# Performance work log

Hardware: AMD Instinct MI355X
Metric: run time of the kernel (lower is better)

## Reference

```python
import jax, jax.numpy as jnp
import numpy as np

N = 2048        # nodes
IN_DIM = 128    # input feature dim
K = 8           # channels
D = 32          # per-channel dim (C_dim)
ITERS = 4       # routing iterations
BETA = 1.0      # attention temperature
EPS = 1e-12     # F.normalize eps


def l2norm(x):
    # F.normalize(x, dim=-1): x / max(||x||_2, eps)
    n = jnp.linalg.norm(x, axis=-1, keepdims=True)
    return x / jnp.maximum(n, EPS)


def setup_inputs() -> dict:
    key = jax.random.key(0)
    k1, k2, k3, k4 = jax.random.split(key, 4)
    adj = jax.random.randint(k1, (N, N), 0, 2, dtype=jnp.int32)
    features = jax.random.normal(k2, (N, IN_DIM), dtype=jnp.float32)
    # parameters initialized ~ N(0,1) as in init_parameters
    W = jax.random.normal(k3, (K, IN_DIM, D), dtype=jnp.float32)
    b = jax.random.normal(k4, (K, D), dtype=jnp.float32)
    return {"adj": adj, "features": features, "W": W, "b": b}


def reference(adj, features, W, b):
    mask = (adj > 0)[None, :, :]                         # [1, N, N]
    # per-channel projection + row L2 normalize -> Z: [K, N, D]
    Z = l2norm(jnp.einsum('nd,kdc->knc', features, W) + b[:, None, :])
    for _ in range(ITERS):
        # per-channel masked attention scores [K, N, N]
        att = jnp.einsum('knc,kmc->knm', Z, Z)
        att = jnp.where(mask, att, 0.0) / BETA
        # softmax across channels (dim=2 in torch after cat == K axis here)
        att = jax.nn.softmax(att, axis=0)
        att = jnp.where(mask, att, 0.0)
        # weighted aggregate + residual + L2 normalize
        Z = l2norm(Z + jnp.einsum('knm,kmc->knc', att, Z))
    # concat channels along feature dim -> [N, K*D]
    return jnp.transpose(Z, (1, 0, 2)).reshape(N, K * D)
```

## Files before the change

### kernel.cpp

```cpp
#include <hip/hip_runtime.h>
#include <hip/hip_bf16.h>
#include <hip/hip_fp16.h>

#define NN 2048
#define KK 8
#define DD 32
#define ZSZ (KK * NN * DD)

#define TW(row, slot) (((row) << 4) + ((((slot) ^ (((row) >> 1) & 3))) << 2))
#define TW2(row, wo) (((row) << 4) + (((((wo) >> 2) ^ (((row) >> 1) & 3))) << 2) + ((wo) & 3))

typedef __attribute__((ext_vector_type(8))) short short8;
typedef __attribute__((ext_vector_type(4))) short short4v;
typedef __attribute__((ext_vector_type(4))) float f32x4;
typedef __attribute__((ext_vector_type(4))) unsigned int u32x4;

union UU { u32x4 q; short8 v; unsigned int u[4]; };
union U2 { uint2 q; short4v v; unsigned int u[2]; };

__device__ __forceinline__ unsigned int bfr(float x) {
  unsigned int u = __float_as_uint(x);
  return (u + 0x7fffu + ((u >> 16) & 1u)) >> 16;
}
__device__ __forceinline__ float bf2f(unsigned int h) {
  return __uint_as_float(h << 16);
}
__device__ __forceinline__ unsigned int packp(float a, float b) {
  union { __hip_bfloat162 h; unsigned int u; } cv;
  cv.h = __float22bfloat162_rn(make_float2(a, b));
  return cv.u;
}
__device__ __forceinline__ f32x4 MF(short8 a, short8 b, f32x4 c) {
  return __builtin_amdgcn_mfma_f32_16x16x32_bf16(a, b, c, 0, 0, 0);
}
__device__ __forceinline__ f32x4 MF16(short4v a, short4v b, f32x4 c) {
  return __builtin_amdgcn_mfma_f32_16x16x16bf16_1k(a, b, c, 0, 0, 0);
}
__device__ __forceinline__ short8 as_s8(u32x4 x) { UU u; u.q = x; return u.v; }

__global__ __launch_bounds__(256) void pm_kernel(const float* __restrict__ feat,
                                                 const float* __restrict__ W,
                                                 const float* __restrict__ bias,
                                                 unsigned short* __restrict__ Zghi,
                                                 unsigned short* __restrict__ Zthi,
                                                 const int* __restrict__ adj,
                                                 unsigned int* __restrict__ mbits) {
  __shared__ float fsh[1024];
  const int t = threadIdx.x;
  if (blockIdx.x < 256) {
    const int nb = blockIdx.x * 8;
    const int k = t >> 5, c = t & 31;
    *(float4*)&fsh[4 * t] = *(const float4*)&feat[nb * 128 + 4 * t];
    float s[8];
#pragma unroll
    for (int j = 0; j < 8; ++j) s[j] = bias[k * DD + c];
    const float* w = W + (k * 128) * DD + c;
    __syncthreads();
#pragma unroll 4
    for (int d = 0; d < 128; ++d) {
      float wv = w[d * DD];
#pragma unroll
      for (int j = 0; j < 8; ++j) s[j] = fmaf(fsh[j * 128 + d], wv, s[j]);
    }
    unsigned int hi[8];
#pragma unroll
    for (int j = 0; j < 8; ++j) {
      float sq = s[j] * s[j];
#pragma unroll
      for (int off = 16; off > 0; off >>= 1) sq += __shfl_xor(sq, off, 32);
      float z = s[j] / fmaxf(sqrtf(sq), 1e-12f);
      hi[j] = bfr(z);
      Zghi[(k * NN + nb + j) * DD + c] = (unsigned short)hi[j];
    }
    uint4 tp = make_uint4(hi[0] | (hi[1] << 16), hi[2] | (hi[3] << 16),
                          hi[4] | (hi[5] << 16), hi[6] | (hi[7] << 16));
    *(uint4*)&Zthi[(size_t)k * DD * NN + (size_t)c * NN + nb] = tp;
  } else {
    const int base = (blockIdx.x - 256) * 1024 + t;
    const int lane = t & 63;
    int v[4];
#pragma unroll
    for (int rr = 0; rr < 4; ++rr) v[rr] = adj[base + 256 * rr];
#pragma unroll
    for (int rr = 0; rr < 4; ++rr) {
      int idx = base + 256 * rr;
      unsigned long long b = __ballot(v[rr] > 0);
      if (lane == 0) mbits[idx >> 5] = (unsigned int)b;
      if (lane == 32) mbits[idx >> 5] = (unsigned int)(b >> 32);
    }
  }
}

template <int NCt>
__global__ __launch_bounds__(256) void rp_kernel(const __half* __restrict__ part,
                                                 unsigned short* __restrict__ Zghi,
                                                 unsigned short* __restrict__ Zthi) {
  __shared__ unsigned short T[DD][33];
  const int t = threadIdx.x;
  const int k = blockIdx.x >> 6, mt = blockIdx.x & 63;
  const int m0 = mt * 32;
  const int mloc = t >> 3, c4 = t & 7;
  const size_t idx = (size_t)(k * NN + m0 + mloc) * DD + 4 * c4;
  uint2 zb = *(const uint2*)&Zghi[idx];
  float4 v;
  v.x = bf2f(zb.x & 0xffffu);
  v.y = __uint_as_float(zb.x & 0xffff0000u);
  v.z = bf2f(zb.y & 0xffffu);
  v.w = __uint_as_float(zb.y & 0xffff0000u);
#pragma unroll
  for (int j = 0; j < NCt; ++j) {
    const __half2* ph = (const __half2*)&part[(size_t)j * ZSZ + idx];
    float2 a = __half22float2(ph[0]);
    float2 b = __half22float2(ph[1]);
    v.x += a.x; v.y += a.y; v.z += b.x; v.w += b.y;
  }
  float sq = v.x * v.x + v.y * v.y + v.z * v.z + v.w * v.w;
  sq += __shfl_xor(sq, 1, 8);
  sq += __shfl_xor(sq, 2, 8);
  sq += __shfl_xor(sq, 4, 8);
  const float sc = 1.0f / fmaxf(sqrtf(sq), 1e-12f);
  float z[4] = {v.x * sc, v.y * sc, v.z * sc, v.w * sc};
  unsigned int hi[4];
#pragma unroll
  for (int e = 0; e < 4; ++e) {
    hi[e] = bfr(z[e]);
    T[4 * c4 + e][mloc] = (unsigned short)hi[e];
  }
  *(uint2*)&Zghi[idx] = make_uint2(hi[0] | (hi[1] << 16), hi[2] | (hi[3] << 16));
  __syncthreads();
  const int cloc = t >> 3, m4 = t & 7;
  unsigned int o0 = (unsigned int)T[cloc][4 * m4 + 0] | ((unsigned int)T[cloc][4 * m4 + 1] << 16);
  unsigned int o1 = (unsigned int)T[cloc][4 * m4 + 2] | ((unsigned int)T[cloc][4 * m4 + 3] << 16);
  *(uint2*)&Zthi[(size_t)k * DD * NN + (size_t)cloc * NN + m0 + 4 * m4] = make_uint2(o0, o1);
}

template <int NS>
__global__ __launch_bounds__(256, 2) void iter_kernel(const unsigned short* __restrict__ Zghi,
                                                      const unsigned short* __restrict__ Zthi,
                                                      const unsigned int* __restrict__ mbits,
                                                      __half* __restrict__ part) {
  __shared__ __align__(16) unsigned int lds[2][8192];
  const int t = threadIdx.x;
  const int w = t >> 6;
  const int lane = t & 63;
  const int l15 = lane & 15;
  const int g = lane >> 4;
  const int nw = blockIdx.x * 64 + w * 16;
  const int mchunk = blockIdx.y * (NS * 32);

  const unsigned int* Zg = (const unsigned int*)Zghi;
  const unsigned int* Zt = (const unsigned int*)Zthi;

  short8 A[KK];
#pragma unroll
  for (int k = 0; k < KK; ++k)
    A[k] = as_s8(*(const u32x4*)&Zg[(size_t)(k * NN + nw + l15) * 16 + 4 * g]);

  unsigned int mword[NS];
#pragma unroll
  for (int q4 = 0; q4 < NS / 4; ++q4) {
    uint4 m4 = *(const uint4*)&mbits[(size_t)(nw + l15) * 64 + (mchunk >> 5) + 4 * q4];
    mword[4 * q4 + 0] = m4.x; mword[4 * q4 + 1] = m4.y;
    mword[4 * q4 + 2] = m4.z; mword[4 * q4 + 3] = m4.w;
  }

  f32x4 O[KK][2];
#pragma unroll
  for (int k = 0; k < KK; ++k)
#pragma unroll
    for (int ch = 0; ch < 2; ++ch) O[k][ch] = {0.0f, 0.0f, 0.0f, 0.0f};

  const int sqd = t & 3;
  const int sr0 = t >> 2;

  u32x4 Lgh[4], Lth[4];
  auto do_loads = [&](int mb) {
#pragma unroll
    for (int j = 0; j < 4; ++j) {
      int r = 64 * j + sr0;
      int k = r >> 5, rm = r & 31;
      Lgh[j] = *(const u32x4*)&Zg[(size_t)k * (NN * 16) + (size_t)(mb + rm) * 16 + sqd * 4];
      Lth[j] = *(const u32x4*)&Zt[(size_t)k * (NN * 16) + (size_t)rm * (NN / 2) + (mb >> 1) + sqd * 4];
    }
  };
  auto wr = [&](int buf) {
#pragma unroll
    for (int j = 0; j < 4; ++j) {
      int r = 64 * j + sr0;
      *(u32x4*)&lds[buf][TW(r, sqd)] = Lgh[j];
      *(u32x4*)&lds[buf][4096 + TW(r, sqd)] = Lth[j];
    }
  };

  do_loads(mchunk);
  wr(0);
  if (NS > 1) do_loads(mchunk + 32);
  __syncthreads();

#pragma unroll
  for (int st = 0; st < NS; ++st) {
    const unsigned int* B = lds[st & 1];
    if (st + 1 < NS) wr((st + 1) & 1);
    if (st + 2 < NS) do_loads(mchunk + (st + 2) * 32);

    const unsigned int mw = mword[st];
#pragma unroll
    for (int sub = 0; sub < 2; ++sub) {
      f32x4 S[KK];
#pragma unroll
      for (int k = 0; k < KK; ++k) {
        u32x4 bh = *(const u32x4*)&B[TW(k * 32 + 16 * sub + l15, g)];
        f32x4 z = {0.0f, 0.0f, 0.0f, 0.0f};
        S[k] = MF(as_s8(bh), A[k], z);
      }
#pragma unroll
      for (int r = 0; r < 4; ++r) {
        float e[KK];
        float sum = 0.0f;
#pragma unroll
        for (int k = 0; k < KK; ++k) { e[k] = __expf(S[k][r]); sum += e[k]; }
        float f = ((mw >> (16 * sub + 4 * g + r)) & 1u) ? __builtin_amdgcn_rcpf(sum) : 0.0f;
#pragma unroll
        for (int k = 0; k < KK; ++k) S[k][r] = e[k] * f;
      }
#pragma unroll
      for (int k = 0; k < KK; ++k) {
        U2 pa;
        pa.u[0] = packp(S[k][0], S[k][1]);
        pa.u[1] = packp(S[k][2], S[k][3]);
#pragma unroll
        for (int ch = 0; ch < 2; ++ch) {
          int row = k * 32 + 16 * ch + l15;
          U2 bv;
          bv.q = *(const uint2*)&B[4096 + TW2(row, 8 * sub + 2 * g)];
          O[k][ch] = MF16(pa.v, bv.v, O[k][ch]);
        }
      }
    }
    __syncthreads();
  }

  __half* dst = part + (size_t)blockIdx.y * ZSZ;
#pragma unroll
  for (int k = 0; k < KK; ++k)
#pragma unroll
    for (int ch = 0; ch < 2; ++ch) {
      f32x4 o = O[k][ch];
#pragma unroll
      for (int r = 0; r < 4; ++r)
        dst[(size_t)(k * NN + nw + 4 * g + r) * DD + 16 * ch + l15] = __float2half_rn(o[r]);
    }
}

template <int NCt>
__global__ __launch_bounds__(256) void ro_kernel(const unsigned short* __restrict__ Zghi,
                                                 const __half* __restrict__ part,
                                                 float* __restrict__ out) {
  const int n = blockIdx.x, t = threadIdx.x;
  const int k = t >> 5, c = t & 31;
  const size_t idx = (size_t)(k * NN + n) * DD + c;
  float v = bf2f((unsigned int)Zghi[idx]);
#pragma unroll
  for (int j = 0; j < NCt; ++j) v += __half2float(part[(size_t)j * ZSZ + idx]);
  float sq = v * v;
#pragma unroll
  for (int off = 16; off > 0; off >>= 1) sq += __shfl_xor(sq, off, 32);
  out[n * (KK * DD) + t] = v / fmaxf(sqrtf(sq), 1e-12f);
}

extern "C" void kernel_launch(void* const* d_in, const int* in_sizes, int n_in,
                              void* d_out, int out_size, void* d_ws, size_t ws_size,
                              hipStream_t stream) {
  const int* adj = (const int*)d_in[0];
  const float* feat = (const float*)d_in[1];
  const float* W = (const float*)d_in[2];
  const float* b = (const float*)d_in[3];
  float* out = (float*)d_out;

  int NC = 16;
  while (NC > 4) {
    size_t need = (size_t)ZSZ * 2 * 2 + (size_t)NN * 64 * 4 + (size_t)NC * ZSZ * 2;
    if (need <= ws_size) break;
    NC >>= 1;
  }

  unsigned short* Zghi = (unsigned short*)d_ws;
  unsigned short* Zthi = Zghi + ZSZ;
  unsigned int* mbits = (unsigned int*)(Zthi + ZSZ);
  __half* part = (__half*)(mbits + NN * 64);

  pm_kernel<<<256 + 4096, 256, 0, stream>>>(feat, W, b, Zghi, Zthi, adj, mbits);

  for (int it = 0; it < 4; ++it) {
    if (NC == 16)
      iter_kernel<4><<<dim3(32, 16), 256, 0, stream>>>(Zghi, Zthi, mbits, part);
    else if (NC == 8)
      iter_kernel<8><<<dim3(32, 8), 256, 0, stream>>>(Zghi, Zthi, mbits, part);
    else
      iter_kernel<16><<<dim3(32, 4), 256, 0, stream>>>(Zghi, Zthi, mbits, part);
    if (it < 3) {
      if (NC == 16)
        rp_kernel<16><<<512, 256, 0, stream>>>(part, Zghi, Zthi);
      else if (NC == 8)
        rp_kernel<8><<<512, 256, 0, stream>>>(part, Zghi, Zthi);
      else
        rp_kernel<4><<<512, 256, 0, stream>>>(part, Zghi, Zthi);
    } else {
      if (NC == 16)
        ro_kernel<16><<<NN, 256, 0, stream>>>(Zghi, part, out);
      else if (NC == 8)
        ro_kernel<8><<<NN, 256, 0, stream>>>(Zghi, part, out);
      else
        ro_kernel<4><<<NN, 256, 0, stream>>>(Zghi, part, out);
    }
  }
}
```

Baseline: 182.0 us.

## Stage Zt via global_load_lds, read Zg directly, and split m-range into more chunks

The transposed Z tile is now copied straight from global into LDS with the async global_load_lds builtin instead of going through registers. The row-major Z operand for the score MFMA is read directly from global/L2 rather than LDS, which halves LDS per block and lets occupancy rise to three blocks per CU. The m dimension is split into 32 chunks of two stages each, raising grid parallelism. The cost is more partial-sum traffic for the reduction kernels to read, and uncached global loads sitting in the inner loop.

```diff
diff --git a/kernel.cpp b/kernel.cpp
--- a/kernel.cpp
+++ b/kernel.cpp
@@ -7,7 +7,6 @@
 #define DD 32
 #define ZSZ (KK * NN * DD)
 
-#define TW(row, slot) (((row) << 4) + ((((slot) ^ (((row) >> 1) & 3))) << 2))
 #define TW2(row, wo) (((row) << 4) + (((((wo) >> 2) ^ (((row) >> 1) & 3))) << 2) + ((wo) & 3))
 
 typedef __attribute__((ext_vector_type(8))) short short8;
@@ -37,6 +36,11 @@
   return __builtin_amdgcn_mfma_f32_16x16x16bf16_1k(a, b, c, 0, 0, 0);
 }
 __device__ __forceinline__ short8 as_s8(u32x4 x) { UU u; u.q = x; return u.v; }
+__device__ __forceinline__ void gl_lds16(const unsigned int* gsrc, unsigned int* ldst) {
+  __builtin_amdgcn_global_load_lds(
+      (const __attribute__((address_space(1))) unsigned int*)gsrc,
+      (__attribute__((address_space(3))) unsigned int*)ldst, 16, 0, 0);
+}
 
 __global__ __launch_bounds__(256) void pm_kernel(const float* __restrict__ feat,
                                                  const float* __restrict__ W,
@@ -135,11 +139,11 @@
 }
 
 template <int NS>
-__global__ __launch_bounds__(256, 2) void iter_kernel(const unsigned short* __restrict__ Zghi,
+__global__ __launch_bounds__(256, 3) void iter_kernel(const unsigned short* __restrict__ Zghi,
                                                       const unsigned short* __restrict__ Zthi,
                                                       const unsigned int* __restrict__ mbits,
                                                       __half* __restrict__ part) {
-  __shared__ __align__(16) unsigned int lds[2][8192];
+  __shared__ __align__(16) unsigned int lds[2][4096];
   const int t = threadIdx.x;
   const int w = t >> 6;
   const int lane = t & 63;
@@ -157,11 +161,16 @@
     A[k] = as_s8(*(const u32x4*)&Zg[(size_t)(k * NN + nw + l15) * 16 + 4 * g]);
 
   unsigned int mword[NS];
-#pragma unroll
-  for (int q4 = 0; q4 < NS / 4; ++q4) {
-    uint4 m4 = *(const uint4*)&mbits[(size_t)(nw + l15) * 64 + (mchunk >> 5) + 4 * q4];
-    mword[4 * q4 + 0] = m4.x; mword[4 * q4 + 1] = m4.y;
-    mword[4 * q4 + 2] = m4.z; mword[4 * q4 + 3] = m4.w;
+  if constexpr (NS == 2) {
+    uint2 m2 = *(const uint2*)&mbits[(size_t)(nw + l15) * 64 + (mchunk >> 5)];
+    mword[0] = m2.x; mword[1] = m2.y;
+  } else {
+#pragma unroll
+    for (int q4 = 0; q4 < NS / 4; ++q4) {
+      uint4 m4 = *(const uint4*)&mbits[(size_t)(nw + l15) * 64 + (mchunk >> 5) + 4 * q4];
+      mword[4 * q4 + 0] = m4.x; mword[4 * q4 + 1] = m4.y;
+      mword[4 * q4 + 2] = m4.z; mword[4 * q4 + 3] = m4.w;
+    }
   }
 
   f32x4 O[KK][2];
@@ -170,46 +179,33 @@
 #pragma unroll
     for (int ch = 0; ch < 2; ++ch) O[k][ch] = {0.0f, 0.0f, 0.0f, 0.0f};
 
-  const int sqd = t & 3;
-  const int sr0 = t >> 2;
-
-  u32x4 Lgh[4], Lth[4];
-  auto do_loads = [&](int mb) {
+  const int sq = (lane & 3) ^ ((lane >> 3) & 3);
+  auto stage = [&](int mb, int buf) {
 #pragma unroll
     for (int j = 0; j < 4; ++j) {
-      int r = 64 * j + sr0;
+      int r = 64 * j + 16 * w + (lane >> 2);
       int k = r >> 5, rm = r & 31;
-      Lgh[j] = *(const u32x4*)&Zg[(size_t)k * (NN * 16) + (size_t)(mb + rm) * 16 + sqd * 4];
-      Lth[j] = *(const u32x4*)&Zt[(size_t)k * (NN * 16) + (size_t)rm * (NN / 2) + (mb >> 1) + sqd * 4];
+      gl_lds16(&Zt[(size_t)k * (NN * 16) + (size_t)rm * (NN / 2) + (mb >> 1) + 4 * sq],
+               &lds[buf][1024 * j + 256 * w]);
     }
   };
-  auto wr = [&](int buf) {
-#pragma unroll
-    for (int j = 0; j < 4; ++j) {
-      int r = 64 * j + sr0;
-      *(u32x4*)&lds[buf][TW(r, sqd)] = Lgh[j];
-      *(u32x4*)&lds[buf][4096 + TW(r, sqd)] = Lth[j];
-    }
-  };
-
-  do_loads(mchunk);
-  wr(0);
-  if (NS > 1) do_loads(mchunk + 32);
+
+  stage(mchunk, 0);
   __syncthreads();
 
 #pragma unroll
   for (int st = 0; st < NS; ++st) {
     const unsigned int* B = lds[st & 1];
-    if (st + 1 < NS) wr((st + 1) & 1);
-    if (st + 2 < NS) do_loads(mchunk + (st + 2) * 32);
-
+    if (st + 1 < NS) stage(mchunk + (st + 1) * 32, (st + 1) & 1);
+    const int mb = mchunk + st * 32;
     const unsigned int mw = mword[st];
+
 #pragma unroll
     for (int sub = 0; sub < 2; ++sub) {
       f32x4 S[KK];
 #pragma unroll
       for (int k = 0; k < KK; ++k) {
-        u32x4 bh = *(const u32x4*)&B[TW(k * 32 + 16 * sub + l15, g)];
+        u32x4 bh = *(const u32x4*)&Zg[(size_t)(k * NN + mb + 16 * sub + l15) * 16 + 4 * g];
         f32x4 z = {0.0f, 0.0f, 0.0f, 0.0f};
         S[k] = MF(as_s8(bh), A[k], z);
       }
@@ -232,7 +228,7 @@
         for (int ch = 0; ch < 2; ++ch) {
           int row = k * 32 + 16 * ch + l15;
           U2 bv;
-          bv.q = *(const uint2*)&B[4096 + TW2(row, 8 * sub + 2 * g)];
+          bv.q = *(const uint2*)&B[TW2(row, 8 * sub + 2 * g)];
           O[k][ch] = MF16(pa.v, bv.v, O[k][ch]);
         }
       }
@@ -277,8 +273,8 @@
   const float* b = (const float*)d_in[3];
   float* out = (float*)d_out;
 
-  int NC = 16;
-  while (NC > 4) {
+  int NC = 32;
+  while (NC > 8) {
     size_t need = (size_t)ZSZ * 2 * 2 + (size_t)NN * 64 * 4 + (size_t)NC * ZSZ * 2;
     if (need <= ws_size) break;
     NC >>= 1;
@@ -292,26 +288,26 @@
   pm_kernel<<<256 + 4096, 256, 0, stream>>>(feat, W, b, Zghi, Zthi, adj, mbits);
 
   for (int it = 0; it < 4; ++it) {
-    if (NC == 16)
+    if (NC == 32)
+      iter_kernel<2><<<dim3(32, 32), 256, 0, stream>>>(Zghi, Zthi, mbits, part);
+    else if (NC == 16)
       iter_kernel<4><<<dim3(32, 16), 256, 0, stream>>>(Zghi, Zthi, mbits, part);
-    else if (NC == 8)
+    else
       iter_kernel<8><<<dim3(32, 8), 256, 0, stream>>>(Zghi, Zthi, mbits, part);
-    else
-      iter_kernel<16><<<dim3(32, 4), 256, 0, stream>>>(Zghi, Zthi, mbits, part);
     if (it < 3) {
-      if (NC == 16)
+      if (NC == 32)
+        rp_kernel<32><<<512, 256, 0, stream>>>(part, Zghi, Zthi);
+      else if (NC == 16)
         rp_kernel<16><<<512, 256, 0, stream>>>(part, Zghi, Zthi);
-      else if (NC == 8)
+      else
         rp_kernel<8><<<512, 256, 0, stream>>>(part, Zghi, Zthi);
+    } else {
+      if (NC == 32)
+        ro_kernel<32><<<NN, 256, 0, stream>>>(Zghi, part, out);
+      else if (NC == 16)
+        ro_kernel<16><<<NN, 256, 0, stream>>>(Zghi, part, out);
       else
-        rp_kernel<4><<<512, 256, 0, stream>>>(part, Zghi, Zthi);
-    } else {
-      if (NC == 16)
-        ro_kernel<16><<<NN, 256, 0, stream>>>(Zghi, part, out);
-      else if (NC == 8)
         ro_kernel<8><<<NN, 256, 0, stream>>>(Zghi, part, out);
-      else
-        ro_kernel<4><<<NN, 256, 0, stream>>>(Zghi, part, out);
-    }
-  }
-}
+    }
+  }
+}
```

After: 209.0 us. 1.15x slower.

## Software-pipeline Gram MFMAs ahead of softmax with triple-buffered Z tiles

Applied to the files above, without the earlier changes.

Restructures the iteration kernel's main loop so the score MFMAs for the next half-tile are issued before the softmax and aggregation of the current one. The Z (Gram operand) tiles move to a triple-buffered LDS ring and the transposed tiles stay double-buffered. The goal is to hide MFMA latency behind the exp/softmax VALU work and to prefetch one stage further ahead. In exchange, LDS use grows from 64KB to 80KB per block and more score registers are live, which may reduce occupancy under the (256,2) launch bounds.

```diff
diff --git a/kernel.cpp b/kernel.cpp
--- a/kernel.cpp
+++ b/kernel.cpp
@@ -139,7 +139,7 @@
                                                       const unsigned short* __restrict__ Zthi,
                                                       const unsigned int* __restrict__ mbits,
                                                       __half* __restrict__ part) {
-  __shared__ __align__(16) unsigned int lds[2][8192];
+  __shared__ __align__(16) unsigned int lds[20480];
   const int t = threadIdx.x;
   const int w = t >> 6;
   const int lane = t & 63;
@@ -174,69 +174,89 @@
   const int sr0 = t >> 2;
 
   u32x4 Lgh[4], Lth[4];
-  auto do_loads = [&](int mb) {
+  auto dl_g = [&](int mb) {
 #pragma unroll
     for (int j = 0; j < 4; ++j) {
       int r = 64 * j + sr0;
       int k = r >> 5, rm = r & 31;
-      Lgh[j] = *(const u32x4*)&Zg[(size_t)k * (NN * 16) + (size_t)(mb + rm) * 16 + sqd * 4];
-      Lth[j] = *(const u32x4*)&Zt[(size_t)k * (NN * 16) + (size_t)rm * (NN / 2) + (mb >> 1) + sqd * 4];
-    }
-  };
-  auto wr = [&](int buf) {
+      Lgh[j] = *(const u32x4*)&Zg[(size_t)(k * NN + mb + rm) * 16 + 4 * sqd];
+    }
+  };
+  auto wr_g = [&](int buf) {
+#pragma unroll
+    for (int j = 0; j < 4; ++j)
+      *(u32x4*)&lds[buf * 4096 + TW(64 * j + sr0, sqd)] = Lgh[j];
+  };
+  auto dl_t = [&](int mb) {
 #pragma unroll
     for (int j = 0; j < 4; ++j) {
       int r = 64 * j + sr0;
-      *(u32x4*)&lds[buf][TW(r, sqd)] = Lgh[j];
-      *(u32x4*)&lds[buf][4096 + TW(r, sqd)] = Lth[j];
-    }
-  };
-
-  do_loads(mchunk);
-  wr(0);
-  if (NS > 1) do_loads(mchunk + 32);
+      int k = r >> 5, rm = r & 31;
+      Lth[j] = *(const u32x4*)&Zt[(size_t)k * (NN * 16) + (size_t)rm * (NN / 2) + (mb >> 1) + 4 * sqd];
+    }
+  };
+  auto wr_t = [&](int buf) {
+#pragma unroll
+    for (int j = 0; j < 4; ++j)
+      *(u32x4*)&lds[12288 + buf * 4096 + TW(64 * j + sr0, sqd)] = Lth[j];
+  };
+
+  auto gram = [&](int gbuf, int sub, f32x4* S) {
+#pragma unroll
+    for (int k = 0; k < KK; ++k) {
+      u32x4 bh = *(const u32x4*)&lds[gbuf * 4096 + TW(k * 32 + 16 * sub + l15, g)];
+      f32x4 z = {0.0f, 0.0f, 0.0f, 0.0f};
+      S[k] = MF(as_s8(bh), A[k], z);
+    }
+  };
+  auto finish = [&](f32x4* S, int tbuf, int sub, unsigned int mw) {
+#pragma unroll
+    for (int r = 0; r < 4; ++r) {
+      float e[KK];
+      float sum = 0.0f;
+#pragma unroll
+      for (int k = 0; k < KK; ++k) { e[k] = __expf(S[k][r]); sum += e[k]; }
+      float f = ((mw >> (16 * sub + 4 * g + r)) & 1u) ? __builtin_amdgcn_rcpf(sum) : 0.0f;
+#pragma unroll
+      for (int k = 0; k < KK; ++k) S[k][r] = e[k] * f;
+    }
+#pragma unroll
+    for (int k = 0; k < KK; ++k) {
+      U2 pa;
+      pa.u[0] = packp(S[k][0], S[k][1]);
+      pa.u[1] = packp(S[k][2], S[k][3]);
+#pragma unroll
+      for (int ch = 0; ch < 2; ++ch) {
+        int row = k * 32 + 16 * ch + l15;
+        U2 bv;
+        bv.q = *(const uint2*)&lds[12288 + tbuf * 4096 + TW2(row, 8 * sub + 2 * g)];
+        O[k][ch] = MF16(pa.v, bv.v, O[k][ch]);
+      }
+    }
+  };
+
+  dl_g(mchunk); wr_g(0);
+  if (NS > 1) { dl_g(mchunk + 32); wr_g(1); }
+  dl_t(mchunk); wr_t(0);
+  if (NS > 2) dl_g(mchunk + 64);
+  if (NS > 1) dl_t(mchunk + 32);
   __syncthreads();
 
+  f32x4 Scur[KK], Snxt[KK];
+  gram(0, 0, Scur);
+
 #pragma unroll
   for (int st = 0; st < NS; ++st) {
-    const unsigned int* B = lds[st & 1];
-    if (st + 1 < NS) wr((st + 1) & 1);
-    if (st + 2 < NS) do_loads(mchunk + (st + 2) * 32);
-
+    if (st + 2 < NS) wr_g((st + 2) % 3);
+    if (st + 1 < NS) wr_t((st + 1) & 1);
+    if (st + 3 < NS) dl_g(mchunk + (st + 3) * 32);
+    if (st + 2 < NS) dl_t(mchunk + (st + 2) * 32);
     const unsigned int mw = mword[st];
-#pragma unroll
-    for (int sub = 0; sub < 2; ++sub) {
-      f32x4 S[KK];
-#pragma unroll
-      for (int k = 0; k < KK; ++k) {
-        u32x4 bh = *(const u32x4*)&B[TW(k * 32 + 16 * sub + l15, g)];
-        f32x4 z = {0.0f, 0.0f, 0.0f, 0.0f};
-        S[k] = MF(as_s8(bh), A[k], z);
-      }
-#pragma unroll
-      for (int r = 0; r < 4; ++r) {
-        float e[KK];
-        float sum = 0.0f;
-#pragma unroll
-        for (int k = 0; k < KK; ++k) { e[k] = __expf(S[k][r]); sum += e[k]; }
-        float f = ((mw >> (16 * sub + 4 * g + r)) & 1u) ? __builtin_amdgcn_rcpf(sum) : 0.0f;
-#pragma unroll
-        for (int k = 0; k < KK; ++k) S[k][r] = e[k] * f;
-      }
-#pragma unroll
-      for (int k = 0; k < KK; ++k) {
-        U2 pa;
-        pa.u[0] = packp(S[k][0], S[k][1]);
-        pa.u[1] = packp(S[k][2], S[k][3]);
-#pragma unroll
-        for (int ch = 0; ch < 2; ++ch) {
-          int row = k * 32 + 16 * ch + l15;
-          U2 bv;
-          bv.q = *(const uint2*)&B[4096 + TW2(row, 8 * sub + 2 * g)];
-          O[k][ch] = MF16(pa.v, bv.v, O[k][ch]);
-        }
-      }
-    }
+
+    gram(st % 3, 1, Snxt);
+    finish(Scur, st & 1, 0, mw);
+    if (st + 1 < NS) gram((st + 1) % 3, 0, Scur);
+    finish(Snxt, st & 1, 1, mw);
     __syncthreads();
   }
 
```

New measurement: 180.4 us. No clear change (-0.9%).
